# Kernel optimization log

Hardware: AMD Instinct MI355X
Metric: run time of the kernel (lower is better)

## Reference

```python
import jax, jax.numpy as jnp
import numpy as np

NUM_CLASSES = 21
ALPHA = 1.0
NEG_POS_RATIO = 3.0
NEG_FOR_HARD = 100.0
B, N = 128, 8732


def setup_inputs() -> dict:
    key = jax.random.key(0)
    k1, k2, k3, k4, k5 = jax.random.split(key, 5)
    loc_pred = jax.random.normal(k1, (B, N, 4), jnp.float32)
    conf_pred = jax.random.normal(k2, (B, N, NUM_CLASSES), jnp.float32)
    # y_true = [loc_targets(4) | one-hot class(NUM_CLASSES) | pos_indicator(1)]
    loc_t = jax.random.normal(k3, (B, N, 4), jnp.float32)
    pos = (jax.random.uniform(k4, (B, N)) < 0.02).astype(jnp.float32)
    labels = jax.random.randint(k5, (B, N), 1, NUM_CLASSES)
    labels = jnp.where(pos > 0, labels, 0)  # negatives -> background class 0
    onehot = jax.nn.one_hot(labels, NUM_CLASSES, dtype=jnp.float32)
    y_true = jnp.concatenate([loc_t, onehot, pos[..., None]], axis=-1)
    return {"y_true": y_true, "loc_pred": loc_pred, "conf_pred": conf_pred}


def reference(y_true, loc_pred, conf_pred):
    num_boxes = y_true.shape[1]
    # conf part of y_pred is softmaxed before the loss (as in the torch code)
    conf = jax.nn.softmax(conf_pred, axis=-1)                    # (B, N, C)
    # cross-entropy with clamp(1e-7) + log, summed over classes
    conf_loss = -jnp.sum(y_true[:, :, 4:-1] * jnp.log(jnp.clip(conf, 1e-7, None)), axis=-1)  # (B, N)
    # smooth-L1 on the 4 loc coords
    d = y_true[:, :, :4] - loc_pred
    ad = jnp.abs(d)
    loc_loss = jnp.sum(jnp.where(ad < 1.0, 0.5 * d * d, ad - 0.5), axis=-1)  # (B, N)

    pos = y_true[:, :, -1]                                       # (B, N)
    pos_loc_loss = jnp.sum(loc_loss * pos, axis=1)               # (B,)
    pos_conf_loss = jnp.sum(conf_loss * pos, axis=1)             # (B,)

    num_pos = jnp.sum(pos, axis=-1)                              # (B,)
    num_neg = jnp.minimum(NEG_POS_RATIO * num_pos, num_boxes - num_pos)
    has_pos = jnp.sum((num_pos > 0).astype(jnp.float32)) > 0
    num_neg_batch = jnp.where(has_pos, jnp.sum(num_neg), jnp.float32(NEG_FOR_HARD))
    k_neg = jnp.floor(num_neg_batch)  # matches int() truncation in torch

    # hard-negative mining: max non-background confidence on negative anchors
    # confs_start=5, confs_end=4+NUM_CLASSES -> softmax classes 1..NUM_CLASSES-1
    max_confs = ((1.0 - pos) * jnp.sum(conf[:, :, 1:NUM_CLASSES], axis=2)).reshape(-1)  # (B*N,)
    order = jnp.argsort(-max_confs)                              # descending, static shape
    sorted_conf_loss = conf_loss.reshape(-1)[order]
    ranks = jnp.arange(max_confs.shape[0], dtype=jnp.float32)
    neg_conf_loss = jnp.sum(jnp.where(ranks < k_neg, sorted_conf_loss, 0.0))

    num_pos_c = jnp.where(num_pos != 0, num_pos, jnp.ones_like(num_pos))
    total = jnp.sum(pos_conf_loss) + neg_conf_loss + ALPHA * jnp.sum(pos_loc_loss)
    return total / jnp.sum(num_pos_c)
```

## Files before the change

### kernel.cpp

```cpp
#include <hip/hip_runtime.h>

#define BATCH 128
#define NBOX 8732
#define NC 21
#define M (BATCH * NBOX)
#define RPB 256
#define NBLK (M / RPB)
#define NREP1 32
#define NREP2 8
#define NB1 1024
#define NB23 2048
#define CLIP_MAX 16.118095651f

struct Ctl {
  float num_pos[BATCH];
  float pos_conf_sum, pos_loc_sum, s_gt, denom;
  unsigned int k_rem, d1, d2, pad;
};

#define OFF_R1C 1024
#define R1SZ    (NREP1 * NB1 * 4)
#define R23SZ   (NREP2 * NB23 * 4)
#define OFF_R1S (OFF_R1C + R1SZ)
#define OFF_R2C (OFF_R1S + R1SZ)
#define OFF_R2S (OFF_R2C + R23SZ)
#define OFF_R3C (OFF_R2S + R23SZ)
#define OFF_R3S (OFF_R3C + R23SZ)
#define OFF_PCP (OFF_R3S + R23SZ)
#define ZERO_BYTES OFF_PCP
#define OFF_PLP (OFF_PCP + 17472)
#define OFF_MC  (OFF_PLP + 17472)
#define OFF_CL  (OFF_MC + M * 4)

__device__ __forceinline__ unsigned int mckey(float mc) {
  unsigned long long K = (unsigned long long)((double)mc * 4294967296.0);
  return (K > 0xFFFFFFFFull) ? 0xFFFFFFFFu : (unsigned int)K;
}

__global__ __launch_bounds__(256) void k_elem(
    const float* __restrict__ yt, const float* __restrict__ lp,
    const float* __restrict__ cp, float* __restrict__ MC,
    float* __restrict__ CL, float* __restrict__ pc_part,
    float* __restrict__ pl_part, unsigned int* __restrict__ rep1c,
    float* __restrict__ rep1s, Ctl* __restrict__ ctl) {
  __shared__ float s_cp[RPB * NC];
  __shared__ float s_loc[RPB * 4];
  __shared__ float s_pos[RPB];
  __shared__ int   s_lab[RPB];
  __shared__ unsigned int hc[NB1];
  __shared__ float hs[NB1];
  __shared__ float sred[16];

  const int tid = threadIdx.x;
  const int bid = blockIdx.x;
  const int e = bid * RPB + tid;

  const float4 lv = ((const float4*)lp)[e];

  for (int i = tid; i < NB1; i += 256) { hc[i] = 0u; hs[i] = 0.f; }

  {
    const float4* gc = (const float4*)(cp + (size_t)bid * RPB * NC);
    float4* sc = (float4*)s_cp;
    for (int i = tid; i < RPB * NC / 4; i += 256) sc[i] = gc[i];
  }
  {
    const float2* gy = (const float2*)(yt + (size_t)bid * RPB * 26);
    for (int i = tid; i < RPB * 13; i += 256) {
      const float2 v = gy[i];
      const int r = i / 13;
      const int jj = 2 * (i - r * 13);
      if (jj == 0)       { s_loc[4 * r] = v.x;     s_loc[4 * r + 1] = v.y; }
      else if (jj == 2)  { s_loc[4 * r + 2] = v.x; s_loc[4 * r + 3] = v.y; }
      else if (jj == 24) { if (v.x > 0.5f) s_lab[r] = 20; s_pos[r] = v.y; }
      else {
        if (v.x > 0.5f) s_lab[r] = jj - 4;
        if (v.y > 0.5f) s_lab[r] = jj - 3;
      }
    }
  }
  __syncthreads();

  const float4 tv = *(const float4*)(s_loc + 4 * tid);
  const float pos = s_pos[tid];
  const int lab = s_lab[tid];

  float ll;
  {
    const float d0 = tv.x - lv.x, d1 = tv.y - lv.y, d2 = tv.z - lv.z, d3 = tv.w - lv.w;
    const float a0 = fabsf(d0), a1 = fabsf(d1), a2 = fabsf(d2), a3 = fabsf(d3);
    ll  = (a0 < 1.f) ? 0.5f * d0 * d0 : a0 - 0.5f;
    ll += (a1 < 1.f) ? 0.5f * d1 * d1 : a1 - 0.5f;
    ll += (a2 < 1.f) ? 0.5f * d2 * d2 : a2 - 0.5f;
    ll += (a3 < 1.f) ? 0.5f * d3 * d3 : a3 - 0.5f;
  }

  const float* c = s_cp + tid * NC;
  float mx = c[0];
#pragma unroll
  for (int j = 1; j < NC; ++j) mx = fmaxf(mx, c[j]);
  float ssum = 0.f, e0 = 0.f;
#pragma unroll
  for (int j = 0; j < NC; ++j) {
    const float ee = __expf(c[j] - mx);
    ssum += ee;
    if (j == 0) e0 = ee;
  }
  const float plogit = c[lab];
  const float cl = fminf(mx + __logf(ssum) - plogit, CLIP_MAX);
  const float mc = (1.f - pos) * ((ssum - e0) / ssum);

  MC[e] = mc;
  CL[e] = cl;
  const unsigned int b1 = mckey(mc) >> 22;
  atomicAdd(&hc[b1], 1u);
  atomicAdd(&hs[b1], cl);

  const int b0 = (bid * RPB) / NBOX;
  float np0 = (e < (b0 + 1) * NBOX) ? pos : 0.f;
  float np1 = pos - np0;
  float tpc = pos * cl, tpl = pos * ll;
#pragma unroll
  for (int off = 32; off > 0; off >>= 1) {
    tpc += __shfl_down(tpc, off);
    tpl += __shfl_down(tpl, off);
    np0 += __shfl_down(np0, off);
    np1 += __shfl_down(np1, off);
  }
  if ((tid & 63) == 0) {
    const int w = tid >> 6;
    sred[w] = tpc; sred[4 + w] = tpl; sred[8 + w] = np0; sred[12 + w] = np1;
  }
  __syncthreads();
  if (tid == 0) {
    pc_part[bid] = sred[0] + sred[1] + sred[2] + sred[3];
    pl_part[bid] = sred[4] + sred[5] + sred[6] + sred[7];
    const float n0 = sred[8] + sred[9] + sred[10] + sred[11];
    const float n1 = sred[12] + sred[13] + sred[14] + sred[15];
    if (n0 != 0.f) atomicAdd(&ctl->num_pos[b0], n0);
    if (n1 != 0.f && b0 + 1 < BATCH) atomicAdd(&ctl->num_pos[b0 + 1], n1);
  }
  unsigned int* rc = rep1c + (bid & (NREP1 - 1)) * NB1;
  float* rs = rep1s + (bid & (NREP1 - 1)) * NB1;
  for (int i = tid; i < NB1; i += 256)
    if (hc[i]) { atomicAdd(&rc[i], hc[i]); atomicAdd(&rs[i], hs[i]); }
}

template <int LEVEL>
__global__ __launch_bounds__(256) void k_hist(
    const float* __restrict__ MC, const float* __restrict__ CL,
    unsigned int* __restrict__ repc, float* __restrict__ reps,
    const Ctl* __restrict__ ctl) {
  __shared__ unsigned int hc[NB23];
  __shared__ float hs[NB23];
  for (int i = threadIdx.x; i < NB23; i += 256) { hc[i] = 0u; hs[i] = 0.f; }
  __syncthreads();
  const unsigned int dd = (LEVEL == 2) ? ctl->d1 : ((ctl->d1 << 11) | ctl->d2);
  const float4* M4 = (const float4*)MC;
  const int n4 = M / 4;
  const int stride = gridDim.x * 256;
  for (int i = blockIdx.x * 256 + threadIdx.x; i < n4; i += stride) {
    const float4 m = M4[i];
    const float mv[4] = {m.x, m.y, m.z, m.w};
#pragma unroll
    for (int q = 0; q < 4; ++q) {
      const unsigned int K = mckey(mv[q]);
      bool match; unsigned int bin;
      if (LEVEL == 2) { match = (K >> 22) == dd; bin = (K >> 11) & 2047u; }
      else            { match = (K >> 11) == dd; bin = K & 2047u; }
      if (match) {
        const float cl = CL[4 * i + q];
        atomicAdd(&hc[bin], 1u);
        atomicAdd(&hs[bin], cl);
      }
    }
  }
  __syncthreads();
  unsigned int* rc = repc + (blockIdx.x & (NREP2 - 1)) * NB23;
  float* rs = reps + (blockIdx.x & (NREP2 - 1)) * NB23;
  for (int i = threadIdx.x; i < NB23; i += 256)
    if (hc[i]) { atomicAdd(&rc[i], hc[i]); atomicAdd(&rs[i], hs[i]); }
}

template <int LEVEL, int NREP, int NBINS>
__global__ __launch_bounds__(1024) void k_scan(
    const unsigned int* __restrict__ repc, const float* __restrict__ reps,
    const float* __restrict__ pc_part, const float* __restrict__ pl_part,
    Ctl* __restrict__ ctl, float* __restrict__ out) {
  __shared__ unsigned int s[2048];
  __shared__ float sf[2048];
  __shared__ float red[16], rn[16], rh[16], rc[16], ra[16], rb[16];
  __shared__ unsigned int kk;
  __shared__ int win;
  const int tid = threadIdx.x;

  unsigned int c0 = 0, c1 = 0;
  float f0 = 0.f, f1 = 0.f;
  for (int r = 0; r < NREP; ++r) {
    c0 += repc[r * NBINS + tid];
    f0 += reps[r * NBINS + tid];
    if (NBINS > 1024) {
      c1 += repc[r * NBINS + tid + 1024];
      f1 += reps[r * NBINS + tid + 1024];
    }
  }
  s[tid] = c0; s[tid + 1024] = c1;
  sf[tid] = f0; sf[tid + 1024] = f1;

  if (LEVEL == 1) {
    const float np = (tid < BATCH) ? ctl->num_pos[tid] : 0.f;
    float nn  = fminf(3.0f * np, (float)NBOX - np);
    float hp  = (np > 0.f) ? 1.f : 0.f;
    float npc = (tid < BATCH) ? ((np != 0.f) ? np : 1.f) : 0.f;
    float a = 0.f, b = 0.f;
    for (int i = tid; i < NBLK; i += 1024) { a += pc_part[i]; b += pl_part[i]; }
#pragma unroll
    for (int off = 32; off > 0; off >>= 1) {
      nn += __shfl_down(nn, off);   hp += __shfl_down(hp, off);
      npc += __shfl_down(npc, off); a += __shfl_down(a, off);
      b += __shfl_down(b, off);
    }
    const int w = tid >> 6;
    if ((tid & 63) == 0) { rn[w] = nn; rh[w] = hp; rc[w] = npc; ra[w] = a; rb[w] = b; }
    __syncthreads();
    if (tid == 0) {
      float tn = 0.f, th = 0.f, tc = 0.f, ta = 0.f, tb = 0.f;
      for (int i = 0; i < 16; ++i) { tn += rn[i]; th += rh[i]; tc += rc[i]; ta += ra[i]; tb += rb[i]; }
      ctl->denom = tc;
      ctl->pos_conf_sum = ta;
      ctl->pos_loc_sum = tb;
      kk = (unsigned int)floorf((th > 0.f) ? tn : 100.0f);
    }
  } else {
    if (tid == 0) kk = ctl->k_rem;
  }
  if (tid == 0) win = -1;
  __syncthreads();

  const unsigned int krem = kk;
  if (krem != 0) {
    for (int off = 1; off < 2048; off <<= 1) {
      const unsigned int v0 = (tid + off < 2048) ? s[tid + off] : 0u;
      const unsigned int v1 = (tid + 1024 + off < 2048) ? s[tid + 1024 + off] : 0u;
      __syncthreads();
      s[tid] += v0;
      s[tid + 1024] += v1;
      __syncthreads();
    }
#pragma unroll
    for (int t = 0; t < 2; ++t) {
      const int i = tid + t * 1024;
      const unsigned int si = s[i];
      const unsigned int sn = (i < 2047) ? s[i + 1] : 0u;
      if (si >= krem && sn < krem) win = i;
    }
    __syncthreads();
    const int b = win;
    float acc = 0.f;
    if (b >= 0) {
      if (tid > b) acc += sf[tid];
      if (tid + 1024 > b) acc += sf[tid + 1024];
    }
#pragma unroll
    for (int off = 32; off > 0; off >>= 1) acc += __shfl_down(acc, off);
    if ((tid & 63) == 0) red[tid >> 6] = acc;
    __syncthreads();
    if (tid == 0 && b >= 0) {
      float tot = 0.f;
      for (int i = 0; i < 16; ++i) tot += red[i];
      const unsigned int above = (b < 2047) ? s[b + 1] : 0u;
      const unsigned int krem2 = krem - above;
      if (LEVEL < 3) {
        ctl->s_gt += tot;
        ctl->k_rem = krem2;
        if (LEVEL == 1) ctl->d1 = (unsigned int)b;
        else            ctl->d2 = (unsigned int)b;
      } else {
        const unsigned int neq = s[b] - above;
        const float tie = (neq > 0) ? sf[b] * ((float)krem2 / (float)neq) : 0.f;
        const float neg = ctl->s_gt + tot + tie;
        out[0] = (ctl->pos_conf_sum + neg + ctl->pos_loc_sum) / ctl->denom;
      }
    }
  } else if (LEVEL == 3 && tid == 0) {
    out[0] = (ctl->pos_conf_sum + ctl->s_gt + ctl->pos_loc_sum) / ctl->denom;
  }
}

extern "C" void kernel_launch(void* const* d_in, const int* in_sizes, int n_in,
                              void* d_out, int out_size, void* d_ws, size_t ws_size,
                              hipStream_t stream) {
  const float* yt = (const float*)d_in[0];
  const float* lp = (const float*)d_in[1];
  const float* cp = (const float*)d_in[2];
  float* out = (float*)d_out;

  char* ws = (char*)d_ws;
  Ctl* ctl = (Ctl*)ws;
  unsigned int* rep1c = (unsigned int*)(ws + OFF_R1C);
  float*        rep1s = (float*)(ws + OFF_R1S);
  unsigned int* rep2c = (unsigned int*)(ws + OFF_R2C);
  float*        rep2s = (float*)(ws + OFF_R2S);
  unsigned int* rep3c = (unsigned int*)(ws + OFF_R3C);
  float*        rep3s = (float*)(ws + OFF_R3S);
  float* pc_part = (float*)(ws + OFF_PCP);
  float* pl_part = (float*)(ws + OFF_PLP);
  float* MC = (float*)(ws + OFF_MC);
  float* CL = (float*)(ws + OFF_CL);

  hipMemsetAsync(ws, 0, ZERO_BYTES, stream);
  k_elem<<<NBLK, 256, 0, stream>>>(yt, lp, cp, MC, CL, pc_part, pl_part,
                                   rep1c, rep1s, ctl);
  k_scan<1, NREP1, NB1><<<1, 1024, 0, stream>>>(rep1c, rep1s, pc_part, pl_part, ctl, out);
  k_hist<2><<<1024, 256, 0, stream>>>(MC, CL, rep2c, rep2s, ctl);
  k_scan<2, NREP2, NB23><<<1, 1024, 0, stream>>>(rep2c, rep2s, pc_part, pl_part, ctl, out);
  k_hist<3><<<1024, 256, 0, stream>>>(MC, CL, rep3c, rep3s, ctl);
  k_scan<3, NREP2, NB23><<<1, 1024, 0, stream>>>(rep3c, rep3s, pc_part, pl_part, ctl, out);
}
```

Before: 302.5 us.

## Fuse scan/histogram stages into one cooperative kernel; load per-thread rows directly

Replaces the five post-processing launches (three single-block scans and two histogram passes) with one cooperative kernel that uses grid-wide syncs between phases. This removes launch gaps and the idle single-block kernels between passes. The element kernel also stops staging conf and y_true through shared memory: each thread loads its own row into registers and computes the target logit as a dot product with the one-hot vector. Strided per-thread row loads may coalesce worse than the old block-wide staged copies, and grid.sync adds its own barrier cost.

```diff
diff --git a/kernel.cpp b/kernel.cpp
--- a/kernel.cpp
+++ b/kernel.cpp
@@ -1,15 +1,18 @@
 #include <hip/hip_runtime.h>
+#include <hip/hip_cooperative_groups.h>
+
+namespace cg = cooperative_groups;
 
 #define BATCH 128
 #define NBOX 8732
 #define NC 21
 #define M (BATCH * NBOX)
-#define RPB 256
-#define NBLK (M / RPB)
+#define NBLK (M / 256)
 #define NREP1 32
 #define NREP2 8
 #define NB1 1024
 #define NB23 2048
+#define PGRID 256
 #define CLIP_MAX 16.118095651f
 
 struct Ctl {
@@ -37,76 +40,64 @@
   return (K > 0xFFFFFFFFull) ? 0xFFFFFFFFu : (unsigned int)K;
 }
 
-__global__ __launch_bounds__(256) void k_elem(
+__global__ __launch_bounds__(256, 4) void k_elem(
     const float* __restrict__ yt, const float* __restrict__ lp,
     const float* __restrict__ cp, float* __restrict__ MC,
     float* __restrict__ CL, float* __restrict__ pc_part,
     float* __restrict__ pl_part, unsigned int* __restrict__ rep1c,
     float* __restrict__ rep1s, Ctl* __restrict__ ctl) {
-  __shared__ float s_cp[RPB * NC];
-  __shared__ float s_loc[RPB * 4];
-  __shared__ float s_pos[RPB];
-  __shared__ int   s_lab[RPB];
   __shared__ unsigned int hc[NB1];
   __shared__ float hs[NB1];
   __shared__ float sred[16];
 
   const int tid = threadIdx.x;
   const int bid = blockIdx.x;
-  const int e = bid * RPB + tid;
+  const int e = bid * 256 + tid;
+
+  for (int i = tid; i < NB1; i += 256) { hc[i] = 0u; hs[i] = 0.f; }
 
   const float4 lv = ((const float4*)lp)[e];
-
-  for (int i = tid; i < NB1; i += 256) { hc[i] = 0u; hs[i] = 0.f; }
-
+  float2 yw[13];
   {
-    const float4* gc = (const float4*)(cp + (size_t)bid * RPB * NC);
-    float4* sc = (float4*)s_cp;
-    for (int i = tid; i < RPB * NC / 4; i += 256) sc[i] = gc[i];
-  }
+    const float2* y2 = (const float2*)(yt + (size_t)e * 26);
+#pragma unroll
+    for (int j = 0; j < 13; ++j) yw[j] = y2[j];
+  }
+  float cv[NC];
   {
-    const float2* gy = (const float2*)(yt + (size_t)bid * RPB * 26);
-    for (int i = tid; i < RPB * 13; i += 256) {
-      const float2 v = gy[i];
-      const int r = i / 13;
-      const int jj = 2 * (i - r * 13);
-      if (jj == 0)       { s_loc[4 * r] = v.x;     s_loc[4 * r + 1] = v.y; }
-      else if (jj == 2)  { s_loc[4 * r + 2] = v.x; s_loc[4 * r + 3] = v.y; }
-      else if (jj == 24) { if (v.x > 0.5f) s_lab[r] = 20; s_pos[r] = v.y; }
-      else {
-        if (v.x > 0.5f) s_lab[r] = jj - 4;
-        if (v.y > 0.5f) s_lab[r] = jj - 3;
-      }
-    }
-  }
-  __syncthreads();
-
-  const float4 tv = *(const float4*)(s_loc + 4 * tid);
-  const float pos = s_pos[tid];
-  const int lab = s_lab[tid];
-
-  float ll;
-  {
-    const float d0 = tv.x - lv.x, d1 = tv.y - lv.y, d2 = tv.z - lv.z, d3 = tv.w - lv.w;
-    const float a0 = fabsf(d0), a1 = fabsf(d1), a2 = fabsf(d2), a3 = fabsf(d3);
-    ll  = (a0 < 1.f) ? 0.5f * d0 * d0 : a0 - 0.5f;
-    ll += (a1 < 1.f) ? 0.5f * d1 * d1 : a1 - 0.5f;
-    ll += (a2 < 1.f) ? 0.5f * d2 * d2 : a2 - 0.5f;
-    ll += (a3 < 1.f) ? 0.5f * d3 * d3 : a3 - 0.5f;
-  }
-
-  const float* c = s_cp + tid * NC;
-  float mx = c[0];
-#pragma unroll
-  for (int j = 1; j < NC; ++j) mx = fmaxf(mx, c[j]);
+    const float* crow = cp + (size_t)e * NC;
+#pragma unroll
+    for (int j = 0; j < NC; ++j) cv[j] = crow[j];
+  }
+  __syncthreads();
+
+  const float pos = yw[12].y;
+
+  const float d0 = yw[0].x - lv.x, d1 = yw[0].y - lv.y;
+  const float d2 = yw[1].x - lv.z, d3 = yw[1].y - lv.w;
+  const float a0 = fabsf(d0), a1 = fabsf(d1), a2 = fabsf(d2), a3 = fabsf(d3);
+  const float ll = ((a0 < 1.f) ? 0.5f * d0 * d0 : a0 - 0.5f)
+                 + ((a1 < 1.f) ? 0.5f * d1 * d1 : a1 - 0.5f)
+                 + ((a2 < 1.f) ? 0.5f * d2 * d2 : a2 - 0.5f)
+                 + ((a3 < 1.f) ? 0.5f * d3 * d3 : a3 - 0.5f);
+
+  float mx = cv[0];
+#pragma unroll
+  for (int j = 1; j < NC; ++j) mx = fmaxf(mx, cv[j]);
+  float plogit = 0.f;
+#pragma unroll
+  for (int j = 0; j < NC; ++j) {
+    const int w = 4 + j;
+    const float oh = (w & 1) ? yw[w >> 1].y : yw[w >> 1].x;
+    plogit = fmaf(oh, cv[j], plogit);
+  }
   float ssum = 0.f, e0 = 0.f;
 #pragma unroll
   for (int j = 0; j < NC; ++j) {
-    const float ee = __expf(c[j] - mx);
+    const float ee = __expf(cv[j] - mx);
     ssum += ee;
     if (j == 0) e0 = ee;
   }
-  const float plogit = c[lab];
   const float cl = fminf(mx + __logf(ssum) - plogit, CLIP_MAX);
   const float mc = (1.f - pos) * ((ssum - e0) / ssum);
 
@@ -116,7 +107,7 @@
   atomicAdd(&hc[b1], 1u);
   atomicAdd(&hs[b1], cl);
 
-  const int b0 = (bid * RPB) / NBOX;
+  const int b0 = (bid << 8) / NBOX;
   float np0 = (e < (b0 + 1) * NBOX) ? pos : 0.f;
   float np1 = pos - np0;
   float tpc = pos * cl, tpl = pos * ll;
@@ -147,19 +138,18 @@
 }
 
 template <int LEVEL>
-__global__ __launch_bounds__(256) void k_hist(
-    const float* __restrict__ MC, const float* __restrict__ CL,
-    unsigned int* __restrict__ repc, float* __restrict__ reps,
-    const Ctl* __restrict__ ctl) {
-  __shared__ unsigned int hc[NB23];
-  __shared__ float hs[NB23];
-  for (int i = threadIdx.x; i < NB23; i += 256) { hc[i] = 0u; hs[i] = 0.f; }
-  __syncthreads();
-  const unsigned int dd = (LEVEL == 2) ? ctl->d1 : ((ctl->d1 << 11) | ctl->d2);
+__device__ void hist_phase(const float* MC, const float* CL,
+                           unsigned int* repc, float* reps,
+                           unsigned int* hc, float* hs,
+                           unsigned int d1v, unsigned int d2v) {
+  const int tid = threadIdx.x;
+  for (int i = tid; i < NB23; i += 1024) { hc[i] = 0u; hs[i] = 0.f; }
+  __syncthreads();
+  const unsigned int dd = (LEVEL == 2) ? d1v : ((d1v << 11) | d2v);
   const float4* M4 = (const float4*)MC;
   const int n4 = M / 4;
-  const int stride = gridDim.x * 256;
-  for (int i = blockIdx.x * 256 + threadIdx.x; i < n4; i += stride) {
+  const int stride = PGRID * 1024;
+  for (int i = blockIdx.x * 1024 + tid; i < n4; i += stride) {
     const float4 m = M4[i];
     const float mv[4] = {m.x, m.y, m.z, m.w};
 #pragma unroll
@@ -168,32 +158,23 @@
       bool match; unsigned int bin;
       if (LEVEL == 2) { match = (K >> 22) == dd; bin = (K >> 11) & 2047u; }
       else            { match = (K >> 11) == dd; bin = K & 2047u; }
-      if (match) {
-        const float cl = CL[4 * i + q];
-        atomicAdd(&hc[bin], 1u);
-        atomicAdd(&hs[bin], cl);
-      }
+      if (match) { atomicAdd(&hc[bin], 1u); atomicAdd(&hs[bin], CL[4 * i + q]); }
     }
   }
   __syncthreads();
   unsigned int* rc = repc + (blockIdx.x & (NREP2 - 1)) * NB23;
   float* rs = reps + (blockIdx.x & (NREP2 - 1)) * NB23;
-  for (int i = threadIdx.x; i < NB23; i += 256)
+  for (int i = tid; i < NB23; i += 1024)
     if (hc[i]) { atomicAdd(&rc[i], hc[i]); atomicAdd(&rs[i], hs[i]); }
 }
 
 template <int LEVEL, int NREP, int NBINS>
-__global__ __launch_bounds__(1024) void k_scan(
-    const unsigned int* __restrict__ repc, const float* __restrict__ reps,
-    const float* __restrict__ pc_part, const float* __restrict__ pl_part,
-    Ctl* __restrict__ ctl, float* __restrict__ out) {
-  __shared__ unsigned int s[2048];
-  __shared__ float sf[2048];
-  __shared__ float red[16], rn[16], rh[16], rc[16], ra[16], rb[16];
-  __shared__ unsigned int kk;
-  __shared__ int win;
+__device__ void scan_phase(unsigned int* s, float* sf, float* rbuf,
+                           unsigned int* kkp, int* winp,
+                           const unsigned int* repc, const float* reps,
+                           const float* pc_part, const float* pl_part,
+                           Ctl* ctl, float* out) {
   const int tid = threadIdx.x;
-
   unsigned int c0 = 0, c1 = 0;
   float f0 = 0.f, f1 = 0.f;
   for (int r = 0; r < NREP; ++r) {
@@ -221,23 +202,29 @@
       b += __shfl_down(b, off);
     }
     const int w = tid >> 6;
-    if ((tid & 63) == 0) { rn[w] = nn; rh[w] = hp; rc[w] = npc; ra[w] = a; rb[w] = b; }
+    if ((tid & 63) == 0) {
+      rbuf[16 + w] = nn; rbuf[32 + w] = hp; rbuf[48 + w] = npc;
+      rbuf[64 + w] = a;  rbuf[80 + w] = b;
+    }
     __syncthreads();
     if (tid == 0) {
       float tn = 0.f, th = 0.f, tc = 0.f, ta = 0.f, tb = 0.f;
-      for (int i = 0; i < 16; ++i) { tn += rn[i]; th += rh[i]; tc += rc[i]; ta += ra[i]; tb += rb[i]; }
+      for (int i = 0; i < 16; ++i) {
+        tn += rbuf[16 + i]; th += rbuf[32 + i]; tc += rbuf[48 + i];
+        ta += rbuf[64 + i]; tb += rbuf[80 + i];
+      }
       ctl->denom = tc;
       ctl->pos_conf_sum = ta;
       ctl->pos_loc_sum = tb;
-      kk = (unsigned int)floorf((th > 0.f) ? tn : 100.0f);
+      *kkp = (unsigned int)floorf((th > 0.f) ? tn : 100.0f);
     }
   } else {
-    if (tid == 0) kk = ctl->k_rem;
-  }
-  if (tid == 0) win = -1;
-  __syncthreads();
-
-  const unsigned int krem = kk;
+    if (tid == 0) *kkp = *(volatile unsigned int*)&ctl->k_rem;
+  }
+  if (tid == 0) *winp = -1;
+  __syncthreads();
+
+  const unsigned int krem = *kkp;
   if (krem != 0) {
     for (int off = 1; off < 2048; off <<= 1) {
       const unsigned int v0 = (tid + off < 2048) ? s[tid + off] : 0u;
@@ -252,10 +239,10 @@
       const int i = tid + t * 1024;
       const unsigned int si = s[i];
       const unsigned int sn = (i < 2047) ? s[i + 1] : 0u;
-      if (si >= krem && sn < krem) win = i;
+      if (si >= krem && sn < krem) *winp = i;
     }
     __syncthreads();
-    const int b = win;
+    const int b = *winp;
     float acc = 0.f;
     if (b >= 0) {
       if (tid > b) acc += sf[tid];
@@ -263,11 +250,11 @@
     }
 #pragma unroll
     for (int off = 32; off > 0; off >>= 1) acc += __shfl_down(acc, off);
-    if ((tid & 63) == 0) red[tid >> 6] = acc;
+    if ((tid & 63) == 0) rbuf[tid >> 6] = acc;
     __syncthreads();
     if (tid == 0 && b >= 0) {
       float tot = 0.f;
-      for (int i = 0; i < 16; ++i) tot += red[i];
+      for (int i = 0; i < 16; ++i) tot += rbuf[i];
       const unsigned int above = (b < 2047) ? s[b + 1] : 0u;
       const unsigned int krem2 = krem - above;
       if (LEVEL < 3) {
@@ -285,6 +272,45 @@
   } else if (LEVEL == 3 && tid == 0) {
     out[0] = (ctl->pos_conf_sum + ctl->s_gt + ctl->pos_loc_sum) / ctl->denom;
   }
+  __syncthreads();
+}
+
+__global__ __launch_bounds__(1024) void k_post(
+    const float* MC, const float* CL,
+    const unsigned int* rep1c, const float* rep1s,
+    unsigned int* rep2c, float* rep2s,
+    unsigned int* rep3c, float* rep3s,
+    const float* pc_part, const float* pl_part,
+    Ctl* ctl, float* out) {
+  __shared__ unsigned int s[2048];
+  __shared__ float sf[2048];
+  __shared__ float rbuf[96];
+  __shared__ unsigned int kk;
+  __shared__ int win;
+  cg::grid_group grid = cg::this_grid();
+
+  if (blockIdx.x == 0)
+    scan_phase<1, NREP1, NB1>(s, sf, rbuf, &kk, &win, rep1c, rep1s,
+                              pc_part, pl_part, ctl, out);
+  grid.sync();
+  {
+    const unsigned int d1v = *(volatile unsigned int*)&ctl->d1;
+    hist_phase<2>(MC, CL, rep2c, rep2s, s, sf, d1v, 0u);
+  }
+  grid.sync();
+  if (blockIdx.x == 0)
+    scan_phase<2, NREP2, NB23>(s, sf, rbuf, &kk, &win, rep2c, rep2s,
+                               pc_part, pl_part, ctl, out);
+  grid.sync();
+  {
+    const unsigned int d1v = *(volatile unsigned int*)&ctl->d1;
+    const unsigned int d2v = *(volatile unsigned int*)&ctl->d2;
+    hist_phase<3>(MC, CL, rep3c, rep3s, s, sf, d1v, d2v);
+  }
+  grid.sync();
+  if (blockIdx.x == 0)
+    scan_phase<3, NREP2, NB23>(s, sf, rbuf, &kk, &win, rep3c, rep3s,
+                               pc_part, pl_part, ctl, out);
 }
 
 extern "C" void kernel_launch(void* const* d_in, const int* in_sizes, int n_in,
@@ -311,9 +337,8 @@
   hipMemsetAsync(ws, 0, ZERO_BYTES, stream);
   k_elem<<<NBLK, 256, 0, stream>>>(yt, lp, cp, MC, CL, pc_part, pl_part,
                                    rep1c, rep1s, ctl);
-  k_scan<1, NREP1, NB1><<<1, 1024, 0, stream>>>(rep1c, rep1s, pc_part, pl_part, ctl, out);
-  k_hist<2><<<1024, 256, 0, stream>>>(MC, CL, rep2c, rep2s, ctl);
-  k_scan<2, NREP2, NB23><<<1, 1024, 0, stream>>>(rep2c, rep2s, pc_part, pl_part, ctl, out);
-  k_hist<3><<<1024, 256, 0, stream>>>(MC, CL, rep3c, rep3s, ctl);
-  k_scan<3, NREP2, NB23><<<1, 1024, 0, stream>>>(rep3c, rep3s, pc_part, pl_part, ctl, out);
-}
+  void* args[] = {&MC, &CL, &rep1c, &rep1s, &rep2c, &rep2s, &rep3c, &rep3s,
+                  &pc_part, &pl_part, &ctl, &out};
+  hipLaunchCooperativeKernel((void*)k_post, dim3(PGRID), dim3(1024), args, 0,
+                             stream);
+}
```

Result: slower. 382.5 us (+26.4%).
